# Kernel optimization log

Hardware: AMD Instinct MI355X
Metric: run time of the kernel (lower is better)

The kernel has to match this reference:

```python
import jax, jax.numpy as jnp
import numpy as np

DIM = 1024
HEADS = 16
ORDER = 3
B, L = 4, 1024  # note: L must equal DIM due to broadcast in original code


def setup_inputs() -> dict:
    key = jax.random.key(0)
    ks = jax.random.split(key, 10)
    D = DIM
    s = 0.02
    inp = {
        "x": jax.random.normal(ks[0], (B, L, D), dtype=jnp.float32),
        "Wq": jax.random.normal(ks[1], (D, D), dtype=jnp.float32) * s,
        "bq": jnp.zeros((D,), jnp.float32),
        "Wk": jax.random.normal(ks[2], (D, D), dtype=jnp.float32) * s,
        "bk": jnp.zeros((D,), jnp.float32),
        "Wv": jax.random.normal(ks[3], (D, D), dtype=jnp.float32) * s,
        "bv": jnp.zeros((D,), jnp.float32),
        "Wo": jax.random.normal(ks[4], (D, D), dtype=jnp.float32) * s,
        "bo": jnp.zeros((D,), jnp.float32),
        # init per module: zeros field, 0.1 strengths
        "torsion_field": jnp.zeros((ORDER, D), jnp.float32),
        "torsion_strength": jnp.ones((ORDER,), jnp.float32) * 0.1,
    }
    return inp


def reference(x, Wq, bq, Wk, bk, Wv, bv, Wo, bo, torsion_field, torsion_strength):
    Bsz, Ln, D = x.shape
    H = HEADS
    hd = D // H

    def proj(W, b):
        y = jnp.einsum('bld,ed->ble', x, W) + b  # Linear: x @ W.T + b
        return y.reshape(Bsz, Ln, H, hd).transpose(0, 2, 1, 3)  # (B,H,L,hd)

    q = proj(Wq, bq)
    k = proj(Wk, bk)
    v = proj(Wv, bv)

    scores = jnp.einsum('bhld,bhmd->bhlm', q, k) / jnp.sqrt(jnp.float32(hd))

    # torsion bias: sum_i strength_i * sin(arange(L)*(i+1)*pi/L) * sigmoid(field_i)
    # (requires L == D for the elementwise product, as in the original)
    pos = jnp.arange(Ln, dtype=jnp.float32)                       # (L,)
    orders = jnp.arange(1, ORDER + 1, dtype=jnp.float32)          # (O,)
    mods = torsion_strength[:, None] * jnp.sin(pos[None, :] * orders[:, None] * jnp.pi / Ln)  # (O,L)
    phases = jax.nn.sigmoid(torsion_field)                        # (O,D), D==L
    bias = jnp.sum(mods * phases, axis=0)                         # (L,)
    scores = scores + bias[None, None, None, :]

    torsion_energy = jnp.sum(torsion_strength ** 2) / ORDER

    attn = jax.nn.softmax(scores, axis=-1)
    out = jnp.einsum('bhlm,bhmd->bhld', attn, v)
    out = out.transpose(0, 2, 1, 3).reshape(Bsz, Ln, D)
    out = jnp.einsum('bld,ed->ble', out, Wo) + bo
    return out, attn, torsion_energy
```

## Files before the change

kernel.cpp:

```cpp
#include <hip/hip_runtime.h>
#include <hip/hip_bf16.h>

typedef __bf16 bf16x8 __attribute__((ext_vector_type(8)));
typedef float f32x4 __attribute__((ext_vector_type(4)));

#define GLDS16(gp, lp) \
    __builtin_amdgcn_global_load_lds((__attribute__((address_space(1))) void*)(gp), \
                                     (__attribute__((address_space(3))) void*)(lp), 16, 0, 0)

static __device__ __forceinline__ void bar_nodrain() {
    __builtin_amdgcn_sched_barrier(0);
    asm volatile("s_waitcnt lgkmcnt(0)" ::: "memory");
    __builtin_amdgcn_s_barrier();
    __builtin_amdgcn_sched_barrier(0);
}

__global__ __launch_bounds__(256) void k_convert(
    const float* __restrict__ x, const float* __restrict__ Wq,
    const float* __restrict__ Wk, const float* __restrict__ Wv,
    const float* __restrict__ Wo,
    __bf16* __restrict__ xb, __bf16* __restrict__ wqb, __bf16* __restrict__ wkb,
    __bf16* __restrict__ wvb, __bf16* __restrict__ wob,
    const float* __restrict__ field, const float* __restrict__ strength,
    float* __restrict__ bias_out, float* __restrict__ energy_out)
{
    if (blockIdx.x == 4096) {
        int t = threadIdx.x;
        #pragma unroll
        for (int m = t; m < 1024; m += 256) {
            float acc = 0.f;
            #pragma unroll
            for (int o = 0; o < 3; ++o) {
                float s  = strength[o];
                float ph = 1.f / (1.f + __expf(-field[o * 1024 + m]));
                float tt = (float)(m * (o + 1)) * 3.14159265358979323846f / 1024.f;
                acc += s * sinf(tt) * ph;
            }
            bias_out[m] = acc;
        }
        if (t == 0) {
            float s0 = strength[0], s1 = strength[1], s2 = strength[2];
            energy_out[0] = (s0 * s0 + s1 * s1 + s2 * s2) * (1.f / 3.f);
        }
        return;
    }
    size_t g = (size_t)blockIdx.x * 256 + threadIdx.x;
    size_t e = g * 8;
    const float* src; __bf16* dst; size_t off;
    if (e < 4194304) { src = x; dst = xb; off = e; }
    else {
        size_t t = e - 4194304;
        int w = (int)(t >> 20); off = t & 1048575;
        src = (w == 0 ? Wq : w == 1 ? Wk : w == 2 ? Wv : Wo);
        dst = (w == 0 ? wqb : w == 1 ? wkb : w == 2 ? wvb : wob);
    }
    float4 a = *(const float4*)(src + off);
    float4 b = *(const float4*)(src + off + 4);
    bf16x8 o;
    o[0] = (__bf16)a.x; o[1] = (__bf16)a.y; o[2] = (__bf16)a.z; o[3] = (__bf16)a.w;
    o[4] = (__bf16)b.x; o[5] = (__bf16)b.y; o[6] = (__bf16)b.z; o[7] = (__bf16)b.w;
    *(bf16x8*)(dst + off) = o;
}

template <int MODE, int BN>
__global__ __launch_bounds__(256) void k_gemm(
    const __bf16* __restrict__ A,
    const __bf16* __restrict__ B0, const __bf16* __restrict__ B1, const __bf16* __restrict__ B2,
    const float* __restrict__ bias0, const float* __restrict__ bias1, const float* __restrict__ bias2,
    __bf16* __restrict__ q_ws, __bf16* __restrict__ k_ws, __bf16* __restrict__ vT_ws,
    float* __restrict__ out)
{
    const int K = 1024;
    constexpr int NB = BN / 32;
    __shared__ __bf16 As[128 * 32];
    __shared__ __bf16 Bs[BN * 32];

    int tid = threadIdx.x;
    int w = tid >> 6, l = tid & 63;
    int l15 = l & 15, quad = l >> 4;
    int m0 = blockIdx.y * 128, n0 = blockIdx.x * BN;
    int z = blockIdx.z;

    const __bf16* Bm = (MODE == 1) ? B0 : (z == 0 ? B0 : (z == 1 ? B1 : B2));
    const float*  bv = (MODE == 1) ? bias0 : (z == 0 ? bias0 : (z == 1 ? bias1 : bias2));

    int srow = w * 16 + (l >> 2);
    int scol = (l & 3) * 8;
    const __bf16* gA = A  + (size_t)(m0 + srow) * K + scol;
    const __bf16* gB = Bm + (size_t)(n0 + srow) * K + scol;
    __bf16* lA = As + w * 512;
    __bf16* lB = Bs + w * 512;

    f32x4 zero = {0.f, 0.f, 0.f, 0.f};
    f32x4 acc[4][NB];
    #pragma unroll
    for (int i = 0; i < 4; ++i)
        #pragma unroll
        for (int j = 0; j < NB; ++j) acc[i][j] = zero;

    int wm = w >> 1, wn = w & 1;

    for (int k0 = 0; k0 < K; k0 += 32) {
        __syncthreads();
        GLDS16(gA + k0,           lA);
        GLDS16(gA + 64 * K + k0,  lA + 2048);
        GLDS16(gB + k0,           lB);
        if (BN == 128) GLDS16(gB + 64 * K + k0,  lB + 2048);
        __builtin_amdgcn_s_waitcnt(0);
        __syncthreads();

        bf16x8 af[4], bfr[NB];
        #pragma unroll
        for (int t = 0; t < 4; ++t)
            af[t] = *(const bf16x8*)&As[(wm * 64 + t * 16 + l15) * 32 + quad * 8];
        #pragma unroll
        for (int t = 0; t < NB; ++t)
            bfr[t] = *(const bf16x8*)&Bs[(wn * (BN / 2) + t * 16 + l15) * 32 + quad * 8];
        #pragma unroll
        for (int i = 0; i < 4; ++i)
            #pragma unroll
            for (int j = 0; j < NB; ++j)
                acc[i][j] = __builtin_amdgcn_mfma_f32_16x16x32_bf16(af[i], bfr[j], acc[i][j], 0, 0, 0);
    }

    #pragma unroll
    for (int i = 0; i < 4; ++i) {
        int mbase = m0 + wm * 64 + i * 16 + quad * 4;
        #pragma unroll
        for (int j = 0; j < NB; ++j) {
            int n = n0 + wn * (BN / 2) + j * 16 + l15;
            float badd = bv[n];
            #pragma unroll
            for (int r = 0; r < 4; ++r) {
                int m = mbase + r;
                float vres = acc[i][j][r] + badd;
                if (MODE == 1) {
                    out[(size_t)m * 1024 + n] = vres;
                } else {
                    int b = m >> 10, lpos = m & 1023, h = n >> 6, d = n & 63;
                    if (z == 2)
                        vT_ws[(((size_t)(b * 16 + h)) * 64 + d) * 1024 + lpos] = (__bf16)vres;
                    else {
                        __bf16* dst = (z == 0 ? q_ws : k_ws);
                        dst[(((size_t)(b * 16 + h)) * 1024 + lpos) * 64 + d] = (__bf16)vres;
                    }
                }
            }
        }
    }
}

__global__ __launch_bounds__(256, 2) void k_attn(
    const __bf16* __restrict__ qg, const __bf16* __restrict__ kg, const __bf16* __restrict__ vTg,
    const float* __restrict__ bias, float* __restrict__ attn, __bf16* __restrict__ Og)
{
    __shared__ __bf16 q_s[128 * 72];
    __shared__ __bf16 K_s[64 * 72];
    __shared__ __bf16 Vt_s[64 * 72];
    __shared__ __bf16 P_s[128 * 72];
    __shared__ float bias_s[1024];
    __shared__ float rowsum[128];
    __shared__ float rowinv[128];

    int tid = threadIdx.x, w = tid >> 6, l = tid & 63;
    int l15 = l & 15, quad = l >> 4;
    int wm = w >> 1, wn = w & 1;
    int bh = blockIdx.y;
    int m0 = blockIdx.x * 128;

    {
        const __bf16* src = qg + ((size_t)bh * 1024 + m0) * 64;
        for (int i = tid; i < 1024; i += 256) {
            int r = i >> 3, c = (i & 7) * 8;
            *(int4*)&q_s[r * 72 + c] = *(const int4*)&src[(size_t)r * 64 + c];
        }
    }
    *(float4*)&bias_s[tid * 4] = *(const float4*)&bias[tid * 4];
    if (tid < 128) rowsum[tid] = 0.f;

    int sr = tid >> 3;
    int sc = (tid & 7) * 8;
    const __bf16* kbase = kg  + (size_t)bh * 1024 * 64;
    const __bf16* vbase = vTg + (size_t)bh * 64 * 1024;

    int4 kr0 = *(const int4*)&kbase[(size_t)(sr)      * 64 + sc];
    int4 kr1 = *(const int4*)&kbase[(size_t)(sr + 32) * 64 + sc];
    int4 vr0 = *(const int4*)&vbase[(size_t)(sr)      * 1024 + sc];
    int4 vr1 = *(const int4*)&vbase[(size_t)(sr + 32) * 1024 + sc];

    f32x4 zero = {0.f, 0.f, 0.f, 0.f};
    f32x4 accO[4][2];
    #pragma unroll
    for (int i = 0; i < 4; ++i) { accO[i][0] = zero; accO[i][1] = zero; }
    float rs[4][4];
    #pragma unroll
    for (int i = 0; i < 4; ++i)
        #pragma unroll
        for (int r = 0; r < 4; ++r) rs[i][r] = 0.f;

    for (int pass = 0; pass < 2; ++pass) {
        for (int ch = 0; ch < 16; ++ch) {
            int n0c = ch * 64;
            bar_nodrain();
            *(int4*)&K_s[sr * 72 + sc]        = kr0;
            *(int4*)&K_s[(sr + 32) * 72 + sc] = kr1;
            if (pass == 0) {
                *(int4*)&Vt_s[sr * 72 + sc]        = vr0;
                *(int4*)&Vt_s[(sr + 32) * 72 + sc] = vr1;
            }
            bar_nodrain();

            if (ch < 15) {
                int nn = n0c + 64;
                kr0 = *(const int4*)&kbase[(size_t)(nn + sr)      * 64 + sc];
                kr1 = *(const int4*)&kbase[(size_t)(nn + sr + 32) * 64 + sc];
                if (pass == 0) {
                    vr0 = *(const int4*)&vbase[(size_t)(sr)      * 1024 + nn + sc];
                    vr1 = *(const int4*)&vbase[(size_t)(sr + 32) * 1024 + nn + sc];
                }
            } else if (pass == 0) {
                kr0 = *(const int4*)&kbase[(size_t)(sr)      * 64 + sc];
                kr1 = *(const int4*)&kbase[(size_t)(sr + 32) * 64 + sc];
            }

            f32x4 accS[4][2];
            #pragma unroll
            for (int i = 0; i < 4; ++i) { accS[i][0] = zero; accS[i][1] = zero; }
            __builtin_amdgcn_s_setprio(1);
            #pragma unroll
            for (int ks2 = 0; ks2 < 2; ++ks2) {
                bf16x8 af[4], bfr[2];
                #pragma unroll
                for (int t = 0; t < 4; ++t)
                    af[t] = *(const bf16x8*)&q_s[(wm * 64 + t * 16 + l15) * 72 + ks2 * 32 + quad * 8];
                #pragma unroll
                for (int t = 0; t < 2; ++t)
                    bfr[t] = *(const bf16x8*)&K_s[(wn * 32 + t * 16 + l15) * 72 + ks2 * 32 + quad * 8];
                #pragma unroll
                for (int i = 0; i < 4; ++i)
                    #pragma unroll
                    for (int j = 0; j < 2; ++j)
                        accS[i][j] = __builtin_amdgcn_mfma_f32_16x16x32_bf16(af[i], bfr[j], accS[i][j], 0, 0, 0);
            }
            __builtin_amdgcn_s_setprio(0);

            float p[4][2][4];
            #pragma unroll
            for (int i = 0; i < 4; ++i)
                #pragma unroll
                for (int j = 0; j < 2; ++j) {
                    float bcol = bias_s[n0c + wn * 32 + j * 16 + l15];
                    #pragma unroll
                    for (int r = 0; r < 4; ++r)
                        p[i][j][r] = __expf(0.125f * accS[i][j][r] + bcol);
                }

            if (pass == 0) {
                #pragma unroll
                for (int i = 0; i < 4; ++i)
                    #pragma unroll
                    for (int r = 0; r < 4; ++r)
                        rs[i][r] += p[i][0][r] + p[i][1][r];
                #pragma unroll
                for (int i = 0; i < 4; ++i)
                    #pragma unroll
                    for (int j = 0; j < 2; ++j)
                        #pragma unroll
                        for (int r = 0; r < 4; ++r)
                            P_s[(wm * 64 + i * 16 + quad * 4 + r) * 72 + wn * 32 + j * 16 + l15] =
                                (__bf16)p[i][j][r];
                bar_nodrain();
                __builtin_amdgcn_s_setprio(1);
                #pragma unroll
                for (int ks2 = 0; ks2 < 2; ++ks2) {
                    bf16x8 af[4], bfr[2];
                    #pragma unroll
                    for (int t = 0; t < 4; ++t)
                        af[t] = *(const bf16x8*)&P_s[(wm * 64 + t * 16 + l15) * 72 + ks2 * 32 + quad * 8];
                    #pragma unroll
                    for (int t = 0; t < 2; ++t)
                        bfr[t] = *(const bf16x8*)&Vt_s[(wn * 32 + t * 16 + l15) * 72 + ks2 * 32 + quad * 8];
                    #pragma unroll
                    for (int i = 0; i < 4; ++i)
                        #pragma unroll
                        for (int j = 0; j < 2; ++j)
                            accO[i][j] = __builtin_amdgcn_mfma_f32_16x16x32_bf16(af[i], bfr[j], accO[i][j], 0, 0, 0);
                }
                __builtin_amdgcn_s_setprio(0);
            } else {
                float* dst = attn + ((size_t)bh << 20) + (size_t)m0 * 1024;
                #pragma unroll
                for (int i = 0; i < 4; ++i)
                    #pragma unroll
                    for (int r = 0; r < 4; ++r) {
                        int row = wm * 64 + i * 16 + quad * 4 + r;
                        float inv = rowinv[row];
                        #pragma unroll
                        for (int j = 0; j < 2; ++j) {
                            int col = n0c + wn * 32 + j * 16 + l15;
                            dst[(size_t)row * 1024 + col] = p[i][j][r] * inv;
                        }
                    }
            }
        }
        if (pass == 0) {
            #pragma unroll
            for (int i = 0; i < 4; ++i)
                #pragma unroll
                for (int r = 0; r < 4; ++r) {
                    float s = rs[i][r];
                    s += __shfl_xor(s, 1, 16);
                    s += __shfl_xor(s, 2, 16);
                    s += __shfl_xor(s, 4, 16);
                    s += __shfl_xor(s, 8, 16);
                    if (l15 == 0) atomicAdd(&rowsum[wm * 64 + i * 16 + quad * 4 + r], s);
                }
            bar_nodrain();
            if (tid < 128) rowinv[tid] = 1.f / rowsum[tid];
            bar_nodrain();
            int b = bh >> 4, h = bh & 15;
            #pragma unroll
            for (int i = 0; i < 4; ++i)
                #pragma unroll
                for (int r = 0; r < 4; ++r) {
                    int row = wm * 64 + i * 16 + quad * 4 + r;
                    float inv = rowinv[row];
                    #pragma unroll
                    for (int j = 0; j < 2; ++j) {
                        int d = wn * 32 + j * 16 + l15;
                        Og[((size_t)(b * 1024 + m0 + row)) * 1024 + h * 64 + d] =
                            (__bf16)(accO[i][j][r] * inv);
                    }
                }
        }
    }
}

extern "C" void kernel_launch(void* const* d_in, const int* in_sizes, int n_in,
                              void* d_out, int out_size, void* d_ws, size_t ws_size,
                              hipStream_t stream)
{
    const float* x  = (const float*)d_in[0];
    const float* Wq = (const float*)d_in[1];
    const float* bq = (const float*)d_in[2];
    const float* Wk = (const float*)d_in[3];
    const float* bk = (const float*)d_in[4];
    const float* Wv = (const float*)d_in[5];
    const float* bvv= (const float*)d_in[6];
    const float* Wo = (const float*)d_in[7];
    const float* bo = (const float*)d_in[8];
    const float* tf = (const float*)d_in[9];
    const float* ts = (const float*)d_in[10];

    float* out    = (float*)d_out;
    float* attn   = out + 4194304;
    float* energy = attn + 67108864;

    char* ws = (char*)d_ws;
    float*  bias  = (float*)ws;
    __bf16* xb    = (__bf16*)(ws + 4096);
    __bf16* wqb   = (__bf16*)(ws + 4096 + 8388608);
    __bf16* wkb   = wqb + 1048576;
    __bf16* wvb   = wkb + 1048576;
    __bf16* wob   = wvb + 1048576;
    __bf16* q_ws  = wob + 1048576;
    __bf16* k_ws  = q_ws + 4194304;
    __bf16* vT_ws = k_ws + 4194304;
    __bf16* O_ws  = xb;

    k_convert<<<dim3(4097), dim3(256), 0, stream>>>(x, Wq, Wk, Wv, Wo, xb, wqb, wkb, wvb, wob,
                                                    tf, ts, bias, energy);
    k_gemm<0, 128><<<dim3(8, 32, 3), dim3(256), 0, stream>>>(xb, wqb, wkb, wvb, bq, bk, bvv,
                                                             q_ws, k_ws, vT_ws, nullptr);
    k_attn<<<dim3(8, 64), dim3(256), 0, stream>>>(q_ws, k_ws, vT_ws, bias, attn, O_ws);
    k_gemm<1, 64><<<dim3(16, 32, 1), dim3(256), 0, stream>>>(O_ws, wob, nullptr, nullptr, bo,
                                                             nullptr, nullptr, nullptr, nullptr,
                                                             nullptr, out);
}
```

Before: 434.0 us.

## Transpose score MFMA for vectorized attn stores and stage V transpose via LDS

The attention kernel now computes S^T (K as the A operand, Q as B), so each lane holds four consecutive key columns for one query row. That allows float4 stores of the attn matrix, float4 bias loads, bf16x4 writes into P_s, and a cheaper row-sum reduction with two shuffles instead of four per row. Separately, the V projection epilogue transposes through a padded LDS tile and writes vT with 16-byte coalesced stores instead of scattered 2-byte stores. This costs extra LDS for the GEMM (about 34KB), which may lower occupancy in the QKV GEMM.

```diff
diff --git a/kernel.cpp b/kernel.cpp
--- a/kernel.cpp
+++ b/kernel.cpp
@@ -2,6 +2,7 @@
 #include <hip/hip_bf16.h>
 
 typedef __bf16 bf16x8 __attribute__((ext_vector_type(8)));
+typedef __bf16 bf16x4 __attribute__((ext_vector_type(4)));
 typedef float f32x4 __attribute__((ext_vector_type(4)));
 
 #define GLDS16(gp, lp) \
@@ -74,6 +75,7 @@
     constexpr int NB = BN / 32;
     __shared__ __bf16 As[128 * 32];
     __shared__ __bf16 Bs[BN * 32];
+    __shared__ __bf16 Cs[MODE == 0 ? 128 * 136 : 4];
 
     int tid = threadIdx.x;
     int w = tid >> 6, l = tid & 63;
@@ -123,6 +125,35 @@
                 acc[i][j] = __builtin_amdgcn_mfma_f32_16x16x32_bf16(af[i], bfr[j], acc[i][j], 0, 0, 0);
     }
 
+    if constexpr (MODE == 0) {
+        if (z == 2) {
+            #pragma unroll
+            for (int j = 0; j < NB; ++j) {
+                int nl = wn * 64 + j * 16 + l15;
+                float badd = bv[n0 + nl];
+                #pragma unroll
+                for (int i = 0; i < 4; ++i) {
+                    int ml = wm * 64 + i * 16 + quad * 4;
+                    bf16x4 cv;
+                    #pragma unroll
+                    for (int r = 0; r < 4; ++r) cv[r] = (__bf16)(acc[i][j][r] + badd);
+                    *(bf16x4*)&Cs[nl * 136 + ml] = cv;
+                }
+            }
+            __syncthreads();
+            int row = tid >> 1;
+            int mh  = (tid & 1) * 64;
+            int n = n0 + row, h = n >> 6, d = n & 63;
+            int b = m0 >> 10;
+            int lpos0 = m0 & 1023;
+            __bf16* drow = vT_ws + (((size_t)(b * 16 + h)) * 64 + d) * 1024 + lpos0 + mh;
+            #pragma unroll
+            for (int s2 = 0; s2 < 8; ++s2)
+                *(int4*)&drow[s2 * 8] = *(const int4*)&Cs[row * 136 + mh + s2 * 8];
+            return;
+        }
+    }
+
     #pragma unroll
     for (int i = 0; i < 4; ++i) {
         int mbase = m0 + wm * 64 + i * 16 + quad * 4;
@@ -138,12 +169,8 @@
                     out[(size_t)m * 1024 + n] = vres;
                 } else {
                     int b = m >> 10, lpos = m & 1023, h = n >> 6, d = n & 63;
-                    if (z == 2)
-                        vT_ws[(((size_t)(b * 16 + h)) * 64 + d) * 1024 + lpos] = (__bf16)vres;
-                    else {
-                        __bf16* dst = (z == 0 ? q_ws : k_ws);
-                        dst[(((size_t)(b * 16 + h)) * 1024 + lpos) * 64 + d] = (__bf16)vres;
-                    }
+                    __bf16* dst = (z == 0 ? q_ws : k_ws);
+                    dst[(((size_t)(b * 16 + h)) * 1024 + lpos) * 64 + d] = (__bf16)vres;
                 }
             }
         }
@@ -192,11 +219,9 @@
     f32x4 accO[4][2];
     #pragma unroll
     for (int i = 0; i < 4; ++i) { accO[i][0] = zero; accO[i][1] = zero; }
-    float rs[4][4];
+    float rs[4];
     #pragma unroll
-    for (int i = 0; i < 4; ++i)
-        #pragma unroll
-        for (int r = 0; r < 4; ++r) rs[i][r] = 0.f;
+    for (int i = 0; i < 4; ++i) rs[i] = 0.f;
 
     for (int pass = 0; pass < 2; ++pass) {
         for (int ch = 0; ch < 16; ++ch) {
@@ -223,63 +248,71 @@
                 kr1 = *(const int4*)&kbase[(size_t)(sr + 32) * 64 + sc];
             }
 
-            f32x4 accS[4][2];
-            #pragma unroll
-            for (int i = 0; i < 4; ++i) { accS[i][0] = zero; accS[i][1] = zero; }
+            f32x4 accT[2][4];
+            #pragma unroll
+            for (int j = 0; j < 2; ++j)
+                #pragma unroll
+                for (int i = 0; i < 4; ++i) accT[j][i] = zero;
             __builtin_amdgcn_s_setprio(1);
             #pragma unroll
             for (int ks2 = 0; ks2 < 2; ++ks2) {
-                bf16x8 af[4], bfr[2];
-                #pragma unroll
-                for (int t = 0; t < 4; ++t)
-                    af[t] = *(const bf16x8*)&q_s[(wm * 64 + t * 16 + l15) * 72 + ks2 * 32 + quad * 8];
-                #pragma unroll
-                for (int t = 0; t < 2; ++t)
-                    bfr[t] = *(const bf16x8*)&K_s[(wn * 32 + t * 16 + l15) * 72 + ks2 * 32 + quad * 8];
-                #pragma unroll
-                for (int i = 0; i < 4; ++i)
-                    #pragma unroll
-                    for (int j = 0; j < 2; ++j)
-                        accS[i][j] = __builtin_amdgcn_mfma_f32_16x16x32_bf16(af[i], bfr[j], accS[i][j], 0, 0, 0);
+                bf16x8 qf[4], kf[2];
+                #pragma unroll
+                for (int t2 = 0; t2 < 4; ++t2)
+                    qf[t2] = *(const bf16x8*)&q_s[(wm * 64 + t2 * 16 + l15) * 72 + ks2 * 32 + quad * 8];
+                #pragma unroll
+                for (int t2 = 0; t2 < 2; ++t2)
+                    kf[t2] = *(const bf16x8*)&K_s[(wn * 32 + t2 * 16 + l15) * 72 + ks2 * 32 + quad * 8];
+                #pragma unroll
+                for (int j = 0; j < 2; ++j)
+                    #pragma unroll
+                    for (int i = 0; i < 4; ++i)
+                        accT[j][i] = __builtin_amdgcn_mfma_f32_16x16x32_bf16(kf[j], qf[i], accT[j][i], 0, 0, 0);
             }
             __builtin_amdgcn_s_setprio(0);
 
+            f32x4 b4[2];
+            #pragma unroll
+            for (int j = 0; j < 2; ++j)
+                b4[j] = *(const f32x4*)&bias_s[n0c + wn * 32 + j * 16 + quad * 4];
+
             float p[4][2][4];
             #pragma unroll
             for (int i = 0; i < 4; ++i)
                 #pragma unroll
-                for (int j = 0; j < 2; ++j) {
-                    float bcol = bias_s[n0c + wn * 32 + j * 16 + l15];
+                for (int j = 0; j < 2; ++j)
                     #pragma unroll
                     for (int r = 0; r < 4; ++r)
-                        p[i][j][r] = __expf(0.125f * accS[i][j][r] + bcol);
-                }
+                        p[i][j][r] = __expf(0.125f * accT[j][i][r] + b4[j][r]);
 
             if (pass == 0) {
-                #pragma unroll
-                for (int i = 0; i < 4; ++i)
-                    #pragma unroll
-                    for (int r = 0; r < 4; ++r)
-                        rs[i][r] += p[i][0][r] + p[i][1][r];
                 #pragma unroll
                 for (int i = 0; i < 4; ++i)
                     #pragma unroll
                     for (int j = 0; j < 2; ++j)
                         #pragma unroll
                         for (int r = 0; r < 4; ++r)
-                            P_s[(wm * 64 + i * 16 + quad * 4 + r) * 72 + wn * 32 + j * 16 + l15] =
-                                (__bf16)p[i][j][r];
+                            rs[i] += p[i][j][r];
+                #pragma unroll
+                for (int i = 0; i < 4; ++i)
+                    #pragma unroll
+                    for (int j = 0; j < 2; ++j) {
+                        bf16x4 pv;
+                        #pragma unroll
+                        for (int r = 0; r < 4; ++r) pv[r] = (__bf16)p[i][j][r];
+                        *(bf16x4*)&P_s[(wm * 64 + i * 16 + l15) * 72 + wn * 32 + j * 16 + quad * 4] = pv;
+                    }
                 bar_nodrain();
                 __builtin_amdgcn_s_setprio(1);
                 #pragma unroll
                 for (int ks2 = 0; ks2 < 2; ++ks2) {
                     bf16x8 af[4], bfr[2];
                     #pragma unroll
-                    for (int t = 0; t < 4; ++t)
-                        af[t] = *(const bf16x8*)&P_s[(wm * 64 + t * 16 + l15) * 72 + ks2 * 32 + quad * 8];
-                    #pragma unroll
-                    for (int t = 0; t < 2; ++t)
-                        bfr[t] = *(const bf16x8*)&Vt_s[(wn * 32 + t * 16 + l15) * 72 + ks2 * 32 + quad * 8];
+                    for (int t2 = 0; t2 < 4; ++t2)
+                        af[t2] = *(const bf16x8*)&P_s[(wm * 64 + t2 * 16 + l15) * 72 + ks2 * 32 + quad * 8];
+                    #pragma unroll
+                    for (int t2 = 0; t2 < 2; ++t2)
+                        bfr[t2] = *(const bf16x8*)&Vt_s[(wn * 32 + t2 * 16 + l15) * 72 + ks2 * 32 + quad * 8];
                     #pragma unroll
                     for (int i = 0; i < 4; ++i)
                         #pragma unroll
@@ -290,31 +323,27 @@
             } else {
                 float* dst = attn + ((size_t)bh << 20) + (size_t)m0 * 1024;
                 #pragma unroll
-                for (int i = 0; i < 4; ++i)
-                    #pragma unroll
-                    for (int r = 0; r < 4; ++r) {
-                        int row = wm * 64 + i * 16 + quad * 4 + r;
-                        float inv = rowinv[row];
-                        #pragma unroll
-                        for (int j = 0; j < 2; ++j) {
-                            int col = n0c + wn * 32 + j * 16 + l15;
-                            dst[(size_t)row * 1024 + col] = p[i][j][r] * inv;
-                        }
+                for (int i = 0; i < 4; ++i) {
+                    int q = wm * 64 + i * 16 + l15;
+                    float inv = rowinv[q];
+                    #pragma unroll
+                    for (int j = 0; j < 2; ++j) {
+                        float4 v;
+                        v.x = p[i][j][0] * inv; v.y = p[i][j][1] * inv;
+                        v.z = p[i][j][2] * inv; v.w = p[i][j][3] * inv;
+                        *(float4*)&dst[(size_t)q * 1024 + n0c + wn * 32 + j * 16 + quad * 4] = v;
                     }
+                }
             }
         }
         if (pass == 0) {
             #pragma unroll
-            for (int i = 0; i < 4; ++i)
-                #pragma unroll
-                for (int r = 0; r < 4; ++r) {
-                    float s = rs[i][r];
-                    s += __shfl_xor(s, 1, 16);
-                    s += __shfl_xor(s, 2, 16);
-                    s += __shfl_xor(s, 4, 16);
-                    s += __shfl_xor(s, 8, 16);
-                    if (l15 == 0) atomicAdd(&rowsum[wm * 64 + i * 16 + quad * 4 + r], s);
-                }
+            for (int i = 0; i < 4; ++i) {
+                float s = rs[i];
+                s += __shfl_xor(s, 16);
+                s += __shfl_xor(s, 32);
+                if (quad == 0) atomicAdd(&rowsum[wm * 64 + i * 16 + l15], s);
+            }
             bar_nodrain();
             if (tid < 128) rowinv[tid] = 1.f / rowsum[tid];
             bar_nodrain();
```

Result: no change. 431.0 us (-0.7%).
